# Kernel optimization log

Measured on AMD Instinct MI355X. Metric: run time of the kernel, lower is better.

## Reference

```python
import jax, jax.numpy as jnp
import numpy as np

N_EMBD = 1024
N_HEAD = 16
HEAD_DIM = N_EMBD // N_HEAD
B, T = 8, 1024


def setup_inputs() -> dict:
    key = jax.random.key(0)
    k1, k2, k3, k4 = jax.random.split(key, 4)
    x = jax.random.normal(k1, (B, T, N_EMBD), dtype=jnp.float32)
    # nn.Linear weight shapes: qkv (3C, C) no bias; proj (C, C) with bias
    w_qkv = jax.random.normal(k2, (3 * N_EMBD, N_EMBD), dtype=jnp.float32) * 0.02
    w_proj = jax.random.normal(k3, (N_EMBD, N_EMBD), dtype=jnp.float32) * 0.02
    b_proj = jax.random.normal(k4, (N_EMBD,), dtype=jnp.float32) * 0.02
    return {"x": x, "w_qkv": w_qkv, "w_proj": w_proj, "b_proj": b_proj}


def reference(x, w_qkv, w_proj, b_proj):
    Bq, Tq, C = x.shape
    qkv = jnp.einsum('btc,dc->btd', x, w_qkv)  # (B,T,3C)
    q, k, v = jnp.split(qkv, 3, axis=-1)
    def heads(t):
        return t.reshape(Bq, Tq, N_HEAD, HEAD_DIM).transpose(0, 2, 1, 3)  # (B,H,T,D)
    q, k, v = heads(q), heads(k), heads(v)
    scale = 1.0 / np.sqrt(HEAD_DIM).astype(np.float32)
    att = jnp.einsum('bhqd,bhkd->bhqk', q, k) * scale  # (B,H,T,T)
    causal = jnp.tril(jnp.ones((Tq, Tq), dtype=bool))
    att = jnp.where(causal, att, -jnp.inf)
    att = jax.nn.softmax(att, axis=-1)
    # dropout: eval mode -> identity
    y = jnp.einsum('bhqk,bhkd->bhqd', att, v)
    y = y.transpose(0, 2, 1, 3).reshape(Bq, Tq, C)
    return jnp.einsum('btc,dc->btd', y, w_proj) + b_proj
```

## Files before the change

kernel.cpp:

```cpp
#include <hip/hip_runtime.h>
#include <stdint.h>


#define Bn 8
#define Tn 1024
#define Cn 1024
#define Hn 16
#define Dn 64
#define Mn (Bn * Tn)
#define NQKV (3 * Cn)

typedef unsigned short u16;
typedef float f32x4 __attribute__((ext_vector_type(4)));
typedef __bf16 bf16x8 __attribute__((ext_vector_type(8)));
typedef unsigned short ushx8 __attribute__((ext_vector_type(8)));
typedef unsigned short ushx4 __attribute__((ext_vector_type(4)));

__device__ __forceinline__ u16 f2bf(float f) {
  unsigned int u = __float_as_uint(f);
  u += 0x7fffu + ((u >> 16) & 1u);
  return (u16)(u >> 16);
}

__device__ __forceinline__ f32x4 mfma_bf16(ushx8 a, ushx8 b, f32x4 c) {
  return __builtin_amdgcn_mfma_f32_16x16x32_bf16(
      __builtin_bit_cast(bf16x8, a), __builtin_bit_cast(bf16x8, b), c, 0, 0, 0);
}

__device__ __forceinline__ void async16(const u16* g, u16* l) {
  __builtin_amdgcn_global_load_lds(
      (__attribute__((address_space(1))) void*)(void*)g,
      (__attribute__((address_space(3))) void*)l, 16, 0, 0);
}

template <int CTRL>
__device__ __forceinline__ float dppmov(float v) {
  return __builtin_bit_cast(float, __builtin_amdgcn_update_dpp(
      0, __builtin_bit_cast(int, v), CTRL, 0xf, 0xf, true));
}
__device__ __forceinline__ float red16max(float v) {
  v = fmaxf(v, dppmov<0xB1>(v));
  v = fmaxf(v, dppmov<0x4E>(v));
  v = fmaxf(v, dppmov<0x141>(v));
  v = fmaxf(v, dppmov<0x140>(v));
  return v;
}
__device__ __forceinline__ float red16sum(float v) {
  v += dppmov<0xB1>(v);
  v += dppmov<0x4E>(v);
  v += dppmov<0x141>(v);
  v += dppmov<0x140>(v);
  return v;
}

__global__ void cast_kernel(const float* __restrict__ in, u16* __restrict__ out, int n4) {
  int i = blockIdx.x * blockDim.x + threadIdx.x;
  if (i < n4) {
    float4 v = ((const float4*)in)[i];
    ushx4 o = { f2bf(v.x), f2bf(v.y), f2bf(v.z), f2bf(v.w) };
    ((ushx4*)out)[i] = o;
  }
}

template <int WRITE_BF16>
__global__ __launch_bounds__(256, 2) void gemm_bt(
    const u16* __restrict__ A, const u16* __restrict__ Bw,
    void* __restrict__ Cout, const float* __restrict__ bias, int N, int K) {
  __shared__ alignas(16) u16 As[128 * 32];
  __shared__ alignas(16) u16 Bs[128 * 32];

  const int tid = threadIdx.x;
  const int lane = tid & 63;
  const int wv = tid >> 6;
  const int quad = lane >> 4;
  const int l16 = lane & 15;
  const int m0 = blockIdx.x * 128;
  const int n0 = blockIdx.y * 128;
  const int wm = (wv >> 1) * 64;
  const int wn = (wv & 1) * 64;

  f32x4 acc[4][4];
#pragma unroll
  for (int i = 0; i < 4; ++i)
#pragma unroll
    for (int j = 0; j < 4; ++j) acc[i][j] = (f32x4){0.f, 0.f, 0.f, 0.f};

  const int r0 = tid >> 2;
  const int cc0 = tid & 3;
  const int gkc0 = cc0 ^ ((r0 >> 1) & 3);
  const int r1 = r0 + 64;
  const int gkc1 = cc0 ^ ((r1 >> 1) & 3);
  const u16* gA0 = A + (size_t)(m0 + r0) * K + gkc0 * 8;
  const u16* gA1 = A + (size_t)(m0 + r1) * K + gkc1 * 8;
  const u16* gB0 = Bw + (size_t)(n0 + r0) * K + gkc0 * 8;
  const u16* gB1 = Bw + (size_t)(n0 + r1) * K + gkc1 * 8;
  u16* lA0 = As + tid * 8;
  u16* lA1 = As + (256 + tid) * 8;
  u16* lB0 = Bs + tid * 8;
  u16* lB1 = Bs + (256 + tid) * 8;

  const u16* pa[4];
  const u16* pb[4];
#pragma unroll
  for (int mi = 0; mi < 4; ++mi) {
    int ra = wm + mi * 16 + l16;
    pa[mi] = As + ra * 32 + (quad ^ ((ra >> 1) & 3)) * 8;
    int rb = wn + mi * 16 + l16;
    pb[mi] = Bs + rb * 32 + (quad ^ ((rb >> 1) & 3)) * 8;
  }

  for (int k0 = 0; k0 < K; k0 += 32) {
    async16(gA0 + k0, lA0);
    async16(gA1 + k0, lA1);
    async16(gB0 + k0, lB0);
    async16(gB1 + k0, lB1);
    __syncthreads();
    ushx8 af[4], bf[4];
#pragma unroll
    for (int i = 0; i < 4; ++i) {
      af[i] = *(const ushx8*)pa[i];
      bf[i] = *(const ushx8*)pb[i];
    }
#pragma unroll
    for (int mi = 0; mi < 4; ++mi)
#pragma unroll
      for (int ni = 0; ni < 4; ++ni)
        acc[mi][ni] = mfma_bf16(af[mi], bf[ni], acc[mi][ni]);
    __syncthreads();
  }

#pragma unroll
  for (int mi = 0; mi < 4; ++mi) {
#pragma unroll
    for (int ni = 0; ni < 4; ++ni) {
      int col = n0 + wn + ni * 16 + l16;
      float bv = 0.f;
      if constexpr (!WRITE_BF16) bv = bias[col];
#pragma unroll
      for (int i = 0; i < 4; ++i) {
        int row = m0 + wm + mi * 16 + quad * 4 + i;
        float v = acc[mi][ni][i] + bv;
        if constexpr (WRITE_BF16)
          ((u16*)Cout)[(size_t)row * N + col] = f2bf(v);
        else
          ((float*)Cout)[(size_t)row * N + col] = v;
      }
    }
  }
}

__global__ __launch_bounds__(256) void transpose_v(
    const u16* __restrict__ qkv, u16* __restrict__ vt) {
  const int t0 = blockIdx.x * 64, h = blockIdx.y, b = blockIdx.z;
  const int lane = threadIdx.x & 63;
  const int wv = threadIdx.x >> 6;
  const u16* vb = qkv + (size_t)b * Tn * NQKV + 2 * Cn + h * Dn + lane;
  u16* ob = vt + ((size_t)(b * Hn + h) * Dn + lane) * Tn + t0;
#pragma unroll
  for (int tc = 0; tc < 2; ++tc) {
    const int t = (wv + tc * 4) * 8;
    ushx8 vals;
#pragma unroll
    for (int e = 0; e < 8; ++e) vals[e] = vb[(size_t)(t0 + t + e) * NQKV];
    *(ushx8*)(ob + t) = vals;
  }
}

#define SLOG2E 0.18033688011112042f

__global__ __launch_bounds__(256, 2) void attn_kernel(
    const u16* __restrict__ qkv, const u16* __restrict__ vt,
    u16* __restrict__ out) {
  const int j = blockIdx.x, h = blockIdx.y, b = blockIdx.z;
  const int tid = threadIdx.x;
  const int lane = tid & 63;
  const int wv = tid >> 6;
  const int quad = lane >> 4;
  const int l16 = lane & 15;

  __shared__ alignas(16) u16 Ks[2][64 * 64];
  __shared__ alignas(16) u16 Vts[2][64 * 64];
  __shared__ alignas(16) u16 Ps[4][32 * 72];

  const u16* qb = qkv + (size_t)b * Tn * NQKV + h * Dn;
  const u16* kb = qkv + (size_t)b * Tn * NQKV + Cn + h * Dn;
  const u16* vtb = vt + (size_t)(b * Hn + h) * Dn * Tn;

  const int srow = tid >> 3;
  const int scc = tid & 7;
  u16* pswv = Ps[wv];

#pragma unroll 1
  for (int ph = 0; ph < 2; ++ph) {
    const int qt = ph ? (7 - j) : j;
    const int q0 = qt * 128;
    const int ntiles = 2 * qt + 2;

    ushx8 qf[2][2];
#pragma unroll
    for (int mi = 0; mi < 2; ++mi) {
      const u16* qp = qb + (size_t)(q0 + wv * 32 + mi * 16 + l16) * NQKV + quad * 8;
      qf[mi][0] = *(const ushx8*)qp;
      qf[mi][1] = *(const ushx8*)(qp + 32);
    }

    f32x4 o[2][4];
#pragma unroll
    for (int mi = 0; mi < 2; ++mi)
#pragma unroll
      for (int nt = 0; nt < 4; ++nt) o[mi][nt] = (f32x4){0.f, 0.f, 0.f, 0.f};
    float mrow[2][4], lrow[2][4];
#pragma unroll
    for (int mi = 0; mi < 2; ++mi)
#pragma unroll
      for (int i = 0; i < 4; ++i) { mrow[mi][i] = -__builtin_inff(); lrow[mi][i] = 0.f; }

    __syncthreads();

#pragma unroll
    for (int c = 0; c < 2; ++c) {
      const int row = c * 32 + srow;
      const int gc = scc ^ (row & 7);
      async16(kb + (size_t)row * NQKV + gc * 8, Ks[0] + (c * 256 + tid) * 8);
      async16(vtb + (size_t)row * Tn + gc * 8, Vts[0] + (c * 256 + tid) * 8);
    }

#pragma unroll 1
    for (int t = 0; t < ntiles; ++t) {
      const int kv0 = t * 64;
      const int bi = t & 1;
      __syncthreads();

      if (t + 1 < ntiles) {
        const int nkv0 = kv0 + 64;
        u16* kd = Ks[bi ^ 1];
        u16* vd = Vts[bi ^ 1];
#pragma unroll
        for (int c = 0; c < 2; ++c) {
          const int row = c * 32 + srow;
          const int gc = scc ^ (row & 7);
          async16(kb + (size_t)(nkv0 + row) * NQKV + gc * 8, kd + (c * 256 + tid) * 8);
          async16(vtb + (size_t)row * Tn + nkv0 + gc * 8, vd + (c * 256 + tid) * 8);
        }
      }

      const u16* ks = Ks[bi];
      const u16* vs = Vts[bi];
      f32x4 s[2][4];
#pragma unroll
      for (int mi = 0; mi < 2; ++mi)
#pragma unroll
        for (int nt = 0; nt < 4; ++nt) s[mi][nt] = (f32x4){0.f, 0.f, 0.f, 0.f};
#pragma unroll
      for (int nt = 0; nt < 4; ++nt) {
        const int rb = nt * 16 + l16;
        ushx8 b0 = *(const ushx8*)(ks + rb * 64 + (quad ^ (rb & 7)) * 8);
        ushx8 b1 = *(const ushx8*)(ks + rb * 64 + ((quad + 4) ^ (rb & 7)) * 8);
#pragma unroll
        for (int mi = 0; mi < 2; ++mi) {
          s[mi][nt] = mfma_bf16(qf[mi][0], b0, s[mi][nt]);
          s[mi][nt] = mfma_bf16(qf[mi][1], b1, s[mi][nt]);
        }
      }

#pragma unroll
      for (int mi = 0; mi < 2; ++mi) {
        const bool dz = (kv0 + 64 > q0 + wv * 32 + mi * 16);
#pragma unroll
        for (int i = 0; i < 4; ++i) {
          const int qr = q0 + wv * 32 + mi * 16 + quad * 4 + i;
          float vv[4];
          float rmax = -__builtin_inff();
#pragma unroll
          for (int nt = 0; nt < 4; ++nt) {
            float v = s[mi][nt][i] * SLOG2E;
            if (dz && (kv0 + nt * 16 + l16) > qr) v = -__builtin_inff();
            vv[nt] = v;
            rmax = fmaxf(rmax, v);
          }
          rmax = red16max(rmax);
          const float mnew = fmaxf(mrow[mi][i], rmax);
          const float al = exp2f(mrow[mi][i] - mnew);
          mrow[mi][i] = mnew;
          float rsum = 0.f;
#pragma unroll
          for (int nt = 0; nt < 4; ++nt) {
            float p = exp2f(vv[nt] - mnew);
            rsum += p;
            pswv[(mi * 16 + quad * 4 + i) * 72 + nt * 16 + l16] = f2bf(p);
          }
          rsum = red16sum(rsum);
          lrow[mi][i] = lrow[mi][i] * al + rsum;
#pragma unroll
          for (int nt = 0; nt < 4; ++nt) o[mi][nt][i] *= al;
        }
      }

      ushx8 pf[2][2];
#pragma unroll
      for (int mi = 0; mi < 2; ++mi) {
        const u16* pp = pswv + (mi * 16 + l16) * 72 + quad * 8;
        pf[mi][0] = *(const ushx8*)pp;
        pf[mi][1] = *(const ushx8*)(pp + 32);
      }

#pragma unroll
      for (int nt = 0; nt < 4; ++nt) {
        const int rb = nt * 16 + l16;
        ushx8 v0 = *(const ushx8*)(vs + rb * 64 + (quad ^ (rb & 7)) * 8);
        ushx8 v1 = *(const ushx8*)(vs + rb * 64 + ((quad + 4) ^ (rb & 7)) * 8);
#pragma unroll
        for (int mi = 0; mi < 2; ++mi) {
          o[mi][nt] = mfma_bf16(pf[mi][0], v0, o[mi][nt]);
          o[mi][nt] = mfma_bf16(pf[mi][1], v1, o[mi][nt]);
        }
      }
    }

#pragma unroll
    for (int mi = 0; mi < 2; ++mi) {
#pragma unroll
      for (int i = 0; i < 4; ++i) {
        const float inv = 1.f / lrow[mi][i];
        const int t = q0 + wv * 32 + mi * 16 + quad * 4 + i;
        u16* op = out + ((size_t)(b * Tn + t)) * Cn + h * Dn + l16;
#pragma unroll
        for (int nt = 0; nt < 4; ++nt) op[nt * 16] = f2bf(o[mi][nt][i] * inv);
      }
    }
  }
}

extern "C" void kernel_launch(void* const* d_in, const int* in_sizes, int n_in,
                              void* d_out, int out_size, void* d_ws, size_t ws_size,
                              hipStream_t stream) {
  const float* x = (const float*)d_in[0];
  const float* w_qkv = (const float*)d_in[1];
  const float* w_proj = (const float*)d_in[2];
  const float* b_proj = (const float*)d_in[3];
  float* out = (float*)d_out;
  char* ws = (char*)d_ws;

  u16* xb     = (u16*)(ws);
  u16* wqkvb  = (u16*)(ws + 16777216);
  u16* wprojb = (u16*)(ws + 23068672);
  u16* qkvb   = (u16*)(ws + 25165824);
  u16* yb     = (u16*)(ws + 75497472);
  u16* vtb    = (u16*)(ws);

  cast_kernel<<<8192, 256, 0, stream>>>(x, xb, 2097152);
  cast_kernel<<<3072, 256, 0, stream>>>(w_qkv, wqkvb, 786432);
  cast_kernel<<<1024, 256, 0, stream>>>(w_proj, wprojb, 262144);

  gemm_bt<1><<<dim3(Mn / 128, NQKV / 128), 256, 0, stream>>>(
      xb, wqkvb, (void*)qkvb, nullptr, NQKV, Cn);

  transpose_v<<<dim3(Tn / 64, Hn, Bn), 256, 0, stream>>>(qkvb, vtb);

  attn_kernel<<<dim3(4, Hn, Bn), 256, 0, stream>>>(qkvb, vtb, yb);

  gemm_bt<0><<<dim3(Mn / 128, Cn / 128), 256, 0, stream>>>(
      yb, wprojb, (void*)out, b_proj, Cn, Cn);
}
```

Baseline: 266.5 us.

## Halve attention query tile, fold softmax scale into QKV GEMM, merge casts

The attention kernel now processes 64-row query tiles (one 16-row slice per wave) with 8 blocks per head instead of 4, doubling grid parallelism and cutting register and LDS use so occupancy can rise to 3 blocks per CU. The softmax scale times log2e is folded into the QKV GEMM epilogue for the Q columns, removing a multiply per score. The code also switches to raw hardware exp2, cheaper round-to-nearest bf16 conversion for P, and one merged cast launch for the three inputs. Smaller query tiles mean K/V tiles are reloaded more often per query row, and rounding of P changes slightly.

```diff
diff --git a/kernel.cpp b/kernel.cpp
--- a/kernel.cpp
+++ b/kernel.cpp
@@ -21,6 +21,9 @@
   u += 0x7fffu + ((u >> 16) & 1u);
   return (u16)(u >> 16);
 }
+__device__ __forceinline__ u16 f2bf_rna(float f) {
+  return (u16)((__float_as_uint(f) + 0x8000u) >> 16);
+}
 
 __device__ __forceinline__ f32x4 mfma_bf16(ushx8 a, ushx8 b, f32x4 c) {
   return __builtin_amdgcn_mfma_f32_16x16x32_bf16(
@@ -53,17 +56,24 @@
   return v;
 }
 
-__global__ void cast_kernel(const float* __restrict__ in, u16* __restrict__ out, int n4) {
+__global__ void cast3_kernel(const float* __restrict__ a, u16* __restrict__ oa, int na4,
+                             const float* __restrict__ b, u16* __restrict__ ob, int nb4,
+                             const float* __restrict__ c, u16* __restrict__ oc, int nc4) {
   int i = blockIdx.x * blockDim.x + threadIdx.x;
-  if (i < n4) {
-    float4 v = ((const float4*)in)[i];
-    ushx4 o = { f2bf(v.x), f2bf(v.y), f2bf(v.z), f2bf(v.w) };
-    ((ushx4*)out)[i] = o;
-  }
-}
-
-template <int WRITE_BF16>
-__global__ __launch_bounds__(256, 2) void gemm_bt(
+  const float* in;
+  u16* out;
+  if (i < na4) { in = a; out = oa; }
+  else if (i < na4 + nb4) { in = b; out = ob; i -= na4; }
+  else if (i < na4 + nb4 + nc4) { in = c; out = oc; i -= na4 + nb4; }
+  else return;
+  float4 v = ((const float4*)in)[i];
+  ushx4 o = { f2bf(v.x), f2bf(v.y), f2bf(v.z), f2bf(v.w) };
+  ((ushx4*)out)[i] = o;
+}
+
+#define SLOG2E 0.18033688011112042f
+template <int WRITE_BF16, int SCALE_Q>
+__global__ __launch_bounds__(256, 3) void gemm_bt(
     const u16* __restrict__ A, const u16* __restrict__ Bw,
     void* __restrict__ Cout, const float* __restrict__ bias, int N, int K) {
   __shared__ alignas(16) u16 As[128 * 32];
@@ -136,10 +146,14 @@
       int col = n0 + wn + ni * 16 + l16;
       float bv = 0.f;
       if constexpr (!WRITE_BF16) bv = bias[col];
+      float sc = 1.f;
+      if constexpr (SCALE_Q) sc = (col < Cn) ? SLOG2E : 1.f;
 #pragma unroll
       for (int i = 0; i < 4; ++i) {
         int row = m0 + wm + mi * 16 + quad * 4 + i;
-        float v = acc[mi][ni][i] + bv;
+        float v = acc[mi][ni][i];
+        if constexpr (SCALE_Q) v *= sc;
+        v += bv;
         if constexpr (WRITE_BF16)
           ((u16*)Cout)[(size_t)row * N + col] = f2bf(v);
         else
@@ -166,9 +180,7 @@
   }
 }
 
-#define SLOG2E 0.18033688011112042f
-
-__global__ __launch_bounds__(256, 2) void attn_kernel(
+__global__ __launch_bounds__(256, 3) void attn_kernel(
     const u16* __restrict__ qkv, const u16* __restrict__ vt,
     u16* __restrict__ out) {
   const int j = blockIdx.x, h = blockIdx.y, b = blockIdx.z;
@@ -180,7 +192,7 @@
 
   __shared__ alignas(16) u16 Ks[2][64 * 64];
   __shared__ alignas(16) u16 Vts[2][64 * 64];
-  __shared__ alignas(16) u16 Ps[4][32 * 72];
+  __shared__ alignas(16) u16 Ps[4][16 * 72];
 
   const u16* qb = qkv + (size_t)b * Tn * NQKV + h * Dn;
   const u16* kb = qkv + (size_t)b * Tn * NQKV + Cn + h * Dn;
@@ -192,28 +204,23 @@
 
 #pragma unroll 1
   for (int ph = 0; ph < 2; ++ph) {
-    const int qt = ph ? (7 - j) : j;
-    const int q0 = qt * 128;
-    const int ntiles = 2 * qt + 2;
-
-    ushx8 qf[2][2];
-#pragma unroll
-    for (int mi = 0; mi < 2; ++mi) {
-      const u16* qp = qb + (size_t)(q0 + wv * 32 + mi * 16 + l16) * NQKV + quad * 8;
-      qf[mi][0] = *(const ushx8*)qp;
-      qf[mi][1] = *(const ushx8*)(qp + 32);
-    }
-
-    f32x4 o[2][4];
-#pragma unroll
-    for (int mi = 0; mi < 2; ++mi)
-#pragma unroll
-      for (int nt = 0; nt < 4; ++nt) o[mi][nt] = (f32x4){0.f, 0.f, 0.f, 0.f};
-    float mrow[2][4], lrow[2][4];
-#pragma unroll
-    for (int mi = 0; mi < 2; ++mi)
-#pragma unroll
-      for (int i = 0; i < 4; ++i) { mrow[mi][i] = -__builtin_inff(); lrow[mi][i] = 0.f; }
+    const int qt = ph ? (15 - j) : j;
+    const int q0 = qt * 64;
+    const int ntiles = qt + 1;
+
+    ushx8 qf[2];
+    {
+      const u16* qp = qb + (size_t)(q0 + wv * 16 + l16) * NQKV + quad * 8;
+      qf[0] = *(const ushx8*)qp;
+      qf[1] = *(const ushx8*)(qp + 32);
+    }
+
+    f32x4 o[4];
+#pragma unroll
+    for (int nt = 0; nt < 4; ++nt) o[nt] = (f32x4){0.f, 0.f, 0.f, 0.f};
+    float mrow[4], lrow[4];
+#pragma unroll
+    for (int i = 0; i < 4; ++i) { mrow[i] = -__builtin_inff(); lrow[i] = 0.f; }
 
     __syncthreads();
 
@@ -246,62 +253,53 @@
 
       const u16* ks = Ks[bi];
       const u16* vs = Vts[bi];
-      f32x4 s[2][4];
-#pragma unroll
-      for (int mi = 0; mi < 2; ++mi)
-#pragma unroll
-        for (int nt = 0; nt < 4; ++nt) s[mi][nt] = (f32x4){0.f, 0.f, 0.f, 0.f};
+      f32x4 s[4];
+#pragma unroll
+      for (int nt = 0; nt < 4; ++nt) s[nt] = (f32x4){0.f, 0.f, 0.f, 0.f};
 #pragma unroll
       for (int nt = 0; nt < 4; ++nt) {
         const int rb = nt * 16 + l16;
         ushx8 b0 = *(const ushx8*)(ks + rb * 64 + (quad ^ (rb & 7)) * 8);
         ushx8 b1 = *(const ushx8*)(ks + rb * 64 + ((quad + 4) ^ (rb & 7)) * 8);
-#pragma unroll
-        for (int mi = 0; mi < 2; ++mi) {
-          s[mi][nt] = mfma_bf16(qf[mi][0], b0, s[mi][nt]);
-          s[mi][nt] = mfma_bf16(qf[mi][1], b1, s[mi][nt]);
+        s[nt] = mfma_bf16(qf[0], b0, s[nt]);
+        s[nt] = mfma_bf16(qf[1], b1, s[nt]);
+      }
+
+      const bool dz = (kv0 + 64 > q0 + wv * 16);
+#pragma unroll
+      for (int i = 0; i < 4; ++i) {
+        const int qr = q0 + wv * 16 + quad * 4 + i;
+        float vv[4];
+        float rmax = -__builtin_inff();
+#pragma unroll
+        for (int nt = 0; nt < 4; ++nt) {
+          float v = s[nt][i];
+          if (dz && (kv0 + nt * 16 + l16) > qr) v = -__builtin_inff();
+          vv[nt] = v;
+          rmax = fmaxf(rmax, v);
         }
-      }
-
-#pragma unroll
-      for (int mi = 0; mi < 2; ++mi) {
-        const bool dz = (kv0 + 64 > q0 + wv * 32 + mi * 16);
-#pragma unroll
-        for (int i = 0; i < 4; ++i) {
-          const int qr = q0 + wv * 32 + mi * 16 + quad * 4 + i;
-          float vv[4];
-          float rmax = -__builtin_inff();
-#pragma unroll
-          for (int nt = 0; nt < 4; ++nt) {
-            float v = s[mi][nt][i] * SLOG2E;
-            if (dz && (kv0 + nt * 16 + l16) > qr) v = -__builtin_inff();
-            vv[nt] = v;
-            rmax = fmaxf(rmax, v);
-          }
-          rmax = red16max(rmax);
-          const float mnew = fmaxf(mrow[mi][i], rmax);
-          const float al = exp2f(mrow[mi][i] - mnew);
-          mrow[mi][i] = mnew;
-          float rsum = 0.f;
-#pragma unroll
-          for (int nt = 0; nt < 4; ++nt) {
-            float p = exp2f(vv[nt] - mnew);
-            rsum += p;
-            pswv[(mi * 16 + quad * 4 + i) * 72 + nt * 16 + l16] = f2bf(p);
-          }
-          rsum = red16sum(rsum);
-          lrow[mi][i] = lrow[mi][i] * al + rsum;
-#pragma unroll
-          for (int nt = 0; nt < 4; ++nt) o[mi][nt][i] *= al;
+        rmax = red16max(rmax);
+        const float mnew = fmaxf(mrow[i], rmax);
+        const float al = __builtin_amdgcn_exp2f(mrow[i] - mnew);
+        mrow[i] = mnew;
+        float rsum = 0.f;
+#pragma unroll
+        for (int nt = 0; nt < 4; ++nt) {
+          float p = __builtin_amdgcn_exp2f(vv[nt] - mnew);
+          rsum += p;
+          pswv[(quad * 4 + i) * 72 + nt * 16 + l16] = f2bf_rna(p);
         }
-      }
-
-      ushx8 pf[2][2];
-#pragma unroll
-      for (int mi = 0; mi < 2; ++mi) {
-        const u16* pp = pswv + (mi * 16 + l16) * 72 + quad * 8;
-        pf[mi][0] = *(const ushx8*)pp;
-        pf[mi][1] = *(const ushx8*)(pp + 32);
+        rsum = red16sum(rsum);
+        lrow[i] = lrow[i] * al + rsum;
+#pragma unroll
+        for (int nt = 0; nt < 4; ++nt) o[nt][i] *= al;
+      }
+
+      ushx8 pf0, pf1;
+      {
+        const u16* pp = pswv + l16 * 72 + quad * 8;
+        pf0 = *(const ushx8*)pp;
+        pf1 = *(const ushx8*)(pp + 32);
       }
 
 #pragma unroll
@@ -309,24 +307,18 @@
         const int rb = nt * 16 + l16;
         ushx8 v0 = *(const ushx8*)(vs + rb * 64 + (quad ^ (rb & 7)) * 8);
         ushx8 v1 = *(const ushx8*)(vs + rb * 64 + ((quad + 4) ^ (rb & 7)) * 8);
-#pragma unroll
-        for (int mi = 0; mi < 2; ++mi) {
-          o[mi][nt] = mfma_bf16(pf[mi][0], v0, o[mi][nt]);
-          o[mi][nt] = mfma_bf16(pf[mi][1], v1, o[mi][nt]);
-        }
-      }
-    }
-
-#pragma unroll
-    for (int mi = 0; mi < 2; ++mi) {
-#pragma unroll
-      for (int i = 0; i < 4; ++i) {
-        const float inv = 1.f / lrow[mi][i];
-        const int t = q0 + wv * 32 + mi * 16 + quad * 4 + i;
-        u16* op = out + ((size_t)(b * Tn + t)) * Cn + h * Dn + l16;
-#pragma unroll
-        for (int nt = 0; nt < 4; ++nt) op[nt * 16] = f2bf(o[mi][nt][i] * inv);
-      }
+        o[nt] = mfma_bf16(pf0, v0, o[nt]);
+        o[nt] = mfma_bf16(pf1, v1, o[nt]);
+      }
+    }
+
+#pragma unroll
+    for (int i = 0; i < 4; ++i) {
+      const float inv = 1.f / lrow[i];
+      const int t = q0 + wv * 16 + quad * 4 + i;
+      u16* op = out + ((size_t)(b * Tn + t)) * Cn + h * Dn + l16;
+#pragma unroll
+      for (int nt = 0; nt < 4; ++nt) op[nt * 16] = f2bf(o[nt][i] * inv);
     }
   }
 }
@@ -348,17 +340,17 @@
   u16* yb     = (u16*)(ws + 75497472);
   u16* vtb    = (u16*)(ws);
 
-  cast_kernel<<<8192, 256, 0, stream>>>(x, xb, 2097152);
-  cast_kernel<<<3072, 256, 0, stream>>>(w_qkv, wqkvb, 786432);
-  cast_kernel<<<1024, 256, 0, stream>>>(w_proj, wprojb, 262144);
-
-  gemm_bt<1><<<dim3(Mn / 128, NQKV / 128), 256, 0, stream>>>(
+  cast3_kernel<<<12288, 256, 0, stream>>>(x, xb, 2097152,
+                                          w_qkv, wqkvb, 786432,
+                                          w_proj, wprojb, 262144);
+
+  gemm_bt<1, 1><<<dim3(Mn / 128, NQKV / 128), 256, 0, stream>>>(
       xb, wqkvb, (void*)qkvb, nullptr, NQKV, Cn);
 
   transpose_v<<<dim3(Tn / 64, Hn, Bn), 256, 0, stream>>>(qkvb, vtb);
 
-  attn_kernel<<<dim3(4, Hn, Bn), 256, 0, stream>>>(qkvb, vtb, yb);
-
-  gemm_bt<0><<<dim3(Mn / 128, Cn / 128), 256, 0, stream>>>(
+  attn_kernel<<<dim3(8, Hn, Bn), 256, 0, stream>>>(qkvb, vtb, yb);
+
+  gemm_bt<0, 0><<<dim3(Mn / 128, Cn / 128), 256, 0, stream>>>(
       yb, wprojb, (void*)out, b_proj, Cn, Cn);
 }
```

After: 252.9 us. 5.1% less time.
